# Kernel optimization log

Measured on AMD Instinct MI355X. Metric: run time of the kernel, lower is better.

The kernel has to match this reference:

```python
import jax, jax.numpy as jnp
import numpy as np

B, N, H, F, K = 64, 64, 256, 8, 2
E = N * (N - 1)


def _lin(k, fan_in, fan_out):
    return jax.random.normal(k, (fan_in, fan_out), jnp.float32) / np.sqrt(fan_in)


def setup_inputs() -> dict:
    key = jax.random.key(0)
    ks = jax.random.split(key, 20)
    # fully-connected directed edge list (no self loops), as in __init__
    idx = np.array([[i, j] for i in range(N) for j in range(N) if i != j], dtype=np.int64).T
    inp = {
        "inputs": jax.random.normal(ks[0], (B, N, F), jnp.float32),
        "hidden": jax.random.normal(ks[1], (B, N, H), jnp.float32),
        "edges": jax.random.uniform(ks[2], (E, K), jnp.float32),
        "edge_index": jnp.asarray(idx),
        # EdgeDecoder MLP: Linear(2H,2H) -> ELU -> Linear(2H,H)
        "ed_w1": _lin(ks[3], 2 * H, 2 * H), "ed_b1": jnp.full((2 * H,), 0.1, jnp.float32),
        "ed_w2": _lin(ks[4], 2 * H, H), "ed_b2": jnp.full((H,), 0.1, jnp.float32),
        # GRU-style hidden linears (no bias)
        "wr": _lin(ks[5], H, H), "wi": _lin(ks[6], H, H), "wh": _lin(ks[7], H, H),
        # input linears (with bias)
        "ir_w": _lin(ks[8], F, H), "ir_b": jnp.full((H,), 0.1, jnp.float32),
        "ii_w": _lin(ks[9], F, H), "ii_b": jnp.full((H,), 0.1, jnp.float32),
        "in_w": _lin(ks[10], F, H), "in_b": jnp.full((H,), 0.1, jnp.float32),
        # output MLP
        "f1_w": _lin(ks[11], H, H), "f1_b": jnp.full((H,), 0.1, jnp.float32),
        "f2_w": _lin(ks[12], H, H), "f2_b": jnp.full((H,), 0.1, jnp.float32),
        "f3_w": _lin(ks[13], H, F), "f3_b": jnp.full((F,), 0.1, jnp.float32),
    }
    return inp


def reference(inputs, hidden, edges, edge_index,
              ed_w1, ed_b1, ed_w2, ed_b2,
              wr, wi, wh,
              ir_w, ir_b, ii_w, ii_b, in_w, in_b,
              f1_w, f1_b, f2_w, f2_b, f3_w, f3_b):
    # convert_edge_index: max over edge-type dim -> per-edge scalar weight [E]
    w = jnp.max(edges, axis=-1)
    src, dst = edge_index[0], edge_index[1]   # PyG: x_j = x[src], x_i = x[dst]
    x_j = hidden[:, src]                      # [B,E,H] gather (irregular)
    x_i = hidden[:, dst]                      # [B,E,H]
    ef = jnp.concatenate([x_i, x_j], axis=-1) * w[None, :, None]   # [B,E,2H]
    # EdgeDecoder.mlp (dropout inactive in eval)
    m = jax.nn.elu(ef @ ed_w1 + ed_b1) @ ed_w2 + ed_b2             # [B,E,H]
    # mean-aggregate messages at receiver nodes (each node has N-1 in-edges)
    agg = jax.ops.segment_sum(m.transpose(1, 0, 2), dst, num_segments=N)
    agg = agg.transpose(1, 0, 2) / (N - 1)                         # [B,N,H]
    # GRU-style update
    r = jax.nn.sigmoid(inputs @ ir_w + ir_b + agg @ wr)
    i = jax.nn.sigmoid(inputs @ ii_w + ii_b + agg @ wi)
    n = jnp.tanh(inputs @ in_w + in_b + r * (agg @ wh))
    new_hidden = (1.0 - i) * n + i * hidden
    # output MLP with residual on inputs (dropout inactive in eval)
    pred = jax.nn.relu(new_hidden @ f1_w + f1_b)
    pred = jax.nn.relu(pred @ f2_w + f2_b)
    pred = inputs + (pred @ f3_w + f3_b)
    return pred, new_hidden
```

## Files before the change

kernel.cpp:

```cpp
#include <hip/hip_runtime.h>
#include <hip/hip_bf16.h>
#include <math.h>

#define BB 64
#define NN 64
#define HH 256
#define FF 8

typedef __bf16 bf16;
typedef bf16 bf16x2 __attribute__((ext_vector_type(2)));
typedef bf16 bf16x4 __attribute__((ext_vector_type(4)));
typedef bf16 bf16x8 __attribute__((ext_vector_type(8)));
typedef float f32x2 __attribute__((ext_vector_type(2)));
typedef float f32x4 __attribute__((ext_vector_type(4)));

#define GLL(g, l) __builtin_amdgcn_global_load_lds( \
    (const __attribute__((address_space(1))) void*)(g), \
    (__attribute__((address_space(3))) void*)(l), 16, 0, 0)

#define MFMA(a, b, c) __builtin_amdgcn_mfma_f32_16x16x32_bf16(a, b, c, 0, 0, 0)

#define WAITVM0 do { asm volatile("s_waitcnt vmcnt(0)" ::: "memory"); \
                     __builtin_amdgcn_sched_barrier(0); } while (0)
#define SBAR __builtin_amdgcn_sched_barrier(0)

__device__ __forceinline__ f32x2 unpk(unsigned int u) {
    union { unsigned int i; float f; } a, b;
    a.i = (u & 0xffffu) << 16;
    b.i = u & 0xffff0000u;
    f32x2 r; r.x = a.f; r.y = b.f; return r;
}

__device__ __forceinline__ bf16x8 frag128(const char* base, int row, int cbyte) {
    const int sw = (row & 7) << 4;
    const int a = row * 128 + cbyte;
    bf16x4 lo = *(const bf16x4*)(base + (a ^ sw));
    bf16x4 hi = *(const bf16x4*)(base + ((a + 32) ^ sw));
    return __builtin_shufflevector(lo, hi, 0, 1, 2, 3, 4, 5, 6, 7);
}

__device__ __forceinline__ bf16x8 frag512(const char* base, int row, int cbyte) {
    const int sw = (row & 7) << 4;
    const int a = row * 512 + cbyte;
    bf16x4 lo = *(const bf16x4*)(base + (a ^ sw));
    bf16x4 hi = *(const bf16x4*)(base + ((a + 32) ^ sw));
    return __builtin_shufflevector(lo, hi, 0, 1, 2, 3, 4, 5, 6, 7);
}

__device__ __forceinline__ bf16x8 frag1024(const char* base, int row, int cbyte) {
    const int sw = (row & 7) << 4;
    const int a = row * 1024 + cbyte;
    bf16x4 lo = *(const bf16x4*)(base + (a ^ sw));
    bf16x4 hi = *(const bf16x4*)(base + ((a + 32) ^ sw));
    return __builtin_shufflevector(lo, hi, 0, 1, 2, 3, 4, 5, 6, 7);
}

__device__ __forceinline__ void st512(char* base, int row, int col, bf16 v) {
    *(bf16*)(base + ((row * 512 + col * 2) ^ ((row & 7) << 4))) = v;
}

__global__ __launch_bounds__(256) void g1pack_kernel(
    const float* __restrict__ hidden, const float* __restrict__ ed_w1,
    const float* __restrict__ ed_w2,
    const float* __restrict__ wr, const float* __restrict__ wi,
    const float* __restrict__ wh,
    const float* __restrict__ f1_w, const float* __restrict__ f2_w,
    bf16* __restrict__ PQ, bf16* __restrict__ W2t, bf16* __restrict__ Wg,
    bf16* __restrict__ f1t, bf16* __restrict__ f2t)
{
    __shared__ __align__(1024) char smem[49408];
    const int tid = threadIdx.x;

    if (blockIdx.y >= 64) {
        const int t = (blockIdx.y - 64) * 16 + blockIdx.x;
        const float* src; bf16* dst; int R, C, tile;
        if (t < 32) { src = ed_w2; dst = W2t; R = 512; C = 256; tile = t; }
        else {
            int m = (t - 32) >> 4; tile = (t - 32) & 15; R = 256; C = 256;
            const float* ss[5] = {wr, wi, wh, f1_w, f2_w};
            bf16* dd[5] = {Wg, Wg + 65536, Wg + 131072, f1t, f2t};
            src = ss[m]; dst = dd[m];
        }
        const int tc = C >> 6;
        const int k0 = (tile / tc) * 64, n0 = (tile % tc) * 64;
        float (*ls)[65] = (float(*)[65])smem;
        {
            int rr = tid >> 2, cc = (tid & 3) * 16;
            const float* sp = src + (size_t)(k0 + rr) * C + n0 + cc;
#pragma unroll
            for (int j = 0; j < 16; j += 4) {
                float4 v = *(const float4*)(sp + j);
                ls[rr][cc + j] = v.x; ls[rr][cc + j + 1] = v.y;
                ls[rr][cc + j + 2] = v.z; ls[rr][cc + j + 3] = v.w;
            }
        }
        __syncthreads();
        {
            int n = tid >> 2, kc = (tid & 3) * 16;
            bf16x8 o0, o1;
#pragma unroll
            for (int j = 0; j < 8; ++j) o0[j] = (bf16)ls[kc + j][n];
#pragma unroll
            for (int j = 0; j < 8; ++j) o1[j] = (bf16)ls[kc + 8 + j][n];
            bf16* dp = dst + (size_t)(n0 + n) * R + k0 + kc;
            *(bf16x8*)dp = o0;
            *(bf16x8*)(dp + 8) = o1;
        }
        return;
    }

    char* Bs = smem;
    char* pool = smem + 32768;
    const int wave = tid >> 6, lane = tid & 63;
    const int wr_ = wave >> 1, wc_ = wave & 1;
    const int l15 = lane & 15, l4 = lane >> 4;
    const int bm = blockIdx.y * 64, bn = blockIdx.x * 64;
    const int roff = (bn >= 512) ? 256 : 0;
    const int ncol = bn & 511;

    {
        float (*ls)[65] = (float(*)[65])pool;
#pragma unroll
        for (int kt = 0; kt < 4; ++kt) {
            {
                int rr = tid >> 2, cc = (tid & 3) * 16;
                const float* sp = ed_w1 + (size_t)(kt * 64 + roff + rr) * 512 + ncol + cc;
#pragma unroll
                for (int j = 0; j < 16; j += 4) {
                    float4 v = *(const float4*)(sp + j);
                    ls[rr][cc + j] = v.x; ls[rr][cc + j + 1] = v.y;
                    ls[rr][cc + j + 2] = v.z; ls[rr][cc + j + 3] = v.w;
                }
            }
            __syncthreads();
            {
                int n = tid >> 2, kc = (tid & 3) * 16;
                bf16x8 o0, o1;
#pragma unroll
                for (int j = 0; j < 8; ++j) o0[j] = (bf16)ls[kc + j][n];
#pragma unroll
                for (int j = 0; j < 8; ++j) o1[j] = (bf16)ls[kc + 8 + j][n];
                int cb0 = kt * 8 + (kc >> 3);
                char* rowp = Bs + n * 512;
                *(bf16x8*)(rowp + ((cb0 ^ (n & 7)) * 16)) = o0;
                *(bf16x8*)(rowp + (((cb0 + 1) ^ (n & 7)) * 16)) = o1;
            }
            __syncthreads();
        }
    }

    f32x4 acc[2][2];
#pragma unroll
    for (int mf = 0; mf < 2; ++mf)
#pragma unroll
        for (int nf = 0; nf < 2; ++nf)
            acc[mf][nf] = (f32x4){0.f, 0.f, 0.f, 0.f};

    auto stageA = [&](int buf, int kt) {
        char* Ab = pool + buf * 8192;
#pragma unroll
        for (int a = 0; a < 2; ++a) {
            int idx = a * 256 + tid;
            int row = idx >> 3, cb = idx & 7;
            const float* gp = hidden + (size_t)(bm + row) * 256 + kt * 64 + cb * 8;
            float4 v0 = *(const float4*)gp;
            float4 v1 = *(const float4*)(gp + 4);
            bf16x8 o;
            o[0] = (bf16)v0.x; o[1] = (bf16)v0.y; o[2] = (bf16)v0.z; o[3] = (bf16)v0.w;
            o[4] = (bf16)v1.x; o[5] = (bf16)v1.y; o[6] = (bf16)v1.z; o[7] = (bf16)v1.w;
            *(bf16x8*)(Ab + row * 128 + ((cb ^ (row & 7)) * 16)) = o;
        }
    };

    auto computeT = [&](int buf, int kt) {
        char* Ab = pool + buf * 8192;
#pragma unroll
        for (int kk = 0; kk < 2; ++kk) {
            bf16x8 af[2];
#pragma unroll
            for (int mf = 0; mf < 2; ++mf)
                af[mf] = frag128(Ab, wr_ * 32 + mf * 16 + l15, kk * 64 + l4 * 8);
#pragma unroll
            for (int nf = 0; nf < 2; ++nf) {
                bf16x8 bfr = frag512(Bs, wc_ * 32 + nf * 16 + l15,
                                     kt * 128 + kk * 64 + l4 * 8);
#pragma unroll
                for (int mf = 0; mf < 2; ++mf)
                    acc[mf][nf] = MFMA(af[mf], bfr, acc[mf][nf]);
            }
        }
    };

    stageA(0, 0);
    __syncthreads();
#pragma unroll
    for (int t = 0; t < 4; ++t) {
        if (t < 3) stageA((t + 1) & 1, t + 1);
        computeT(t & 1, t);
        __syncthreads();
    }

#pragma unroll
    for (int mf = 0; mf < 2; ++mf)
#pragma unroll
        for (int nf = 0; nf < 2; ++nf)
#pragma unroll
            for (int r = 0; r < 4; ++r) {
                int grow = bm + wr_ * 32 + mf * 16 + l4 * 4 + r;
                int col = bn + wc_ * 32 + nf * 16 + l15;
                PQ[(size_t)grow * 1024 + col] = (bf16)acc[mf][nf][r];
            }
}

__global__ __launch_bounds__(1024) void fused_kernel(
    const bf16* __restrict__ PQ, const float* __restrict__ edges,
    const float* __restrict__ b1,
    const bf16* __restrict__ W2t, const float* __restrict__ ed_b2,
    const bf16* __restrict__ Wg,
    const bf16* __restrict__ f1t, const float* __restrict__ f1_b,
    const bf16* __restrict__ f2t, const float* __restrict__ f2_b,
    const float* __restrict__ f3_w, const float* __restrict__ f3_b,
    const float* __restrict__ inputs, const float* __restrict__ hidden,
    const float* __restrict__ irw, const float* __restrict__ irb,
    const float* __restrict__ iiw, const float* __restrict__ iib,
    const float* __restrict__ inw, const float* __restrict__ inb,
    float* __restrict__ NH, float* __restrict__ pred)
{
    __shared__ __align__(1024) char smem[65536];
    char* qs   = smem;
    char* bbase = smem;
    char* sl   = smem + 32768;
    float* f3s = (float*)(smem + 32768);
    char* h1l  = smem + 40960;
    float (*wls)[16] = (float(*)[16])(smem + 49152);
    char* aggl = smem + 49152;
    char* h2l  = smem + 49152;
    char* nhl  = smem + 57344;

    const int tid = threadIdx.x;
    const int wave = tid >> 6, lane = tid & 63;
    const int l15 = lane & 15, l4 = lane >> 4;
    const int srow = lane >> 3;
    const int scol = ((lane & 7) ^ (lane >> 3)) * 8;
    const int vb = (blockIdx.x & 7) * 32 + (blockIdx.x >> 3);
    const int b = vb >> 2, d0 = (vb & 3) * 16;
    const bf16* Pb = PQ + (size_t)(b * 64) * 1024;
    char* mybuf = bbase + wave * 2048;
    const int n0 = wave * 16;

    auto stageB = [&](const bf16* Wt, int Krow, int kt) {
#pragma unroll
        for (int s = 0; s < 2; ++s)
            GLL(Wt + (size_t)(n0 + s * 8 + srow) * Krow + kt * 64 + scol,
                mybuf + s * 1024 + lane * 16);
    };

#pragma unroll
    for (int si = 0; si < 2; ++si) {
        int row = wave * 2 + si;
        GLL(Pb + (size_t)row * 1024 + 512 + lane * 8, qs + row * 1024 + lane * 16);
    }
    {
        int src = tid >> 4, dc = tid & 15, d = d0 + dc;
        float w = 0.f;
        if (src != d) {
            int e = src * 63 + (d < src ? d : d - 1);
            float2 ev = ((const float2*)edges)[e];
            w = fmaxf(ev.x, ev.y);
        }
        wls[src][dc] = w;
    }
    const int c = tid & 255, hh = tid >> 8;
    f32x2 p2[4];
#pragma unroll
    for (int dd = 0; dd < 4; ++dd)
        p2[dd] = unpk(*(const unsigned int*)(Pb + (size_t)(d0 + hh * 4 + dd) * 1024 + 2 * c));
    float2 bbl = *(const float2*)(b1 + 2 * c);
    f32x2 bb; bb.x = bbl.x; bb.y = bbl.y;
    __syncthreads();

    f32x2 acc[4];
#pragma unroll
    for (int dd = 0; dd < 4; ++dd) acc[dd] = (f32x2){0.f, 0.f};
    const unsigned int* Qs32 = (const unsigned int*)qs;
    {
#pragma unroll 4
        for (int src = 0; src < 32; ++src) {
            f32x2 qv = unpk(Qs32[src * 256 + c]);
            float4 wv = *(const float4*)&wls[src][hh * 4];
            float w[4] = {wv.x, wv.y, wv.z, wv.w};
#pragma unroll
            for (int dd = 0; dd < 4; ++dd) {
                f32x2 w2v; w2v.x = w[dd]; w2v.y = w[dd];
                f32x2 v = (p2[dd] + qv) * w2v + bb;
                float e0 = __expf(v.x) - 1.f;
                float e1 = __expf(v.y) - 1.f;
                f32x2 r;
                r.x = (v.x > 0.f) ? v.x : e0;
                r.y = (v.y > 0.f) ? v.y : e1;
                acc[dd] += r;
            }
        }
    }
    __syncthreads();
#pragma unroll
    for (int si = 0; si < 2; ++si) {
        int row = wave * 2 + si;
        GLL(Pb + (size_t)(32 + row) * 1024 + 512 + lane * 8,
            qs + row * 1024 + lane * 16);
    }
    __syncthreads();
    {
#pragma unroll 4
        for (int src = 32; src < 64; ++src) {
            f32x2 qv = unpk(Qs32[(src - 32) * 256 + c]);
            float4 wv = *(const float4*)&wls[src][hh * 4];
            float w[4] = {wv.x, wv.y, wv.z, wv.w};
#pragma unroll
            for (int dd = 0; dd < 4; ++dd) {
                f32x2 w2v; w2v.x = w[dd]; w2v.y = w[dd];
                f32x2 v = (p2[dd] + qv) * w2v + bb;
                float e0 = __expf(v.x) - 1.f;
                float e1 = __expf(v.y) - 1.f;
                f32x2 r;
                r.x = (v.x > 0.f) ? v.x : e0;
                r.y = (v.y > 0.f) ? v.y : e1;
                acc[dd] += r;
            }
        }
        f32x2 selfc;
        selfc.x = (bb.x > 0.f) ? bb.x : (__expf(bb.x) - 1.f);
        selfc.y = (bb.y > 0.f) ? bb.y : (__expf(bb.y) - 1.f);
#pragma unroll
        for (int dd = 0; dd < 4; ++dd) {
            int row = hh * 4 + dd;
            bf16x2 st;
            st[0] = (bf16)(acc[dd].x - selfc.x);
            st[1] = (bf16)(acc[dd].y - selfc.y);
            *(bf16x2*)(sl + ((row * 1024 + 4 * c) ^ ((row & 7) << 4))) = st;
        }
    }
    __syncthreads();

    {
        f32x4 a1 = (f32x4){0.f, 0.f, 0.f, 0.f};
#pragma unroll
        for (int kt = 0; kt < 8; ++kt) {
            SBAR; stageB(W2t, 512, kt); WAITVM0;
#pragma unroll
            for (int kk = 0; kk < 2; ++kk) {
                bf16x8 af = frag1024(sl, l15, kt * 128 + kk * 64 + l4 * 8);
                a1 = MFMA(af, frag128(mybuf, l15, kk * 64 + l4 * 8), a1);
            }
        }
        int col = n0 + l15;
        float eb = ed_b2[col];
#pragma unroll
        for (int r = 0; r < 4; ++r)
            st512(aggl, l4 * 4 + r, col, (bf16)(a1[r] * (1.f / 63.f) + eb));
    }
    __syncthreads();

    for (int i = tid; i < 2048; i += 1024) f3s[i] = f3_w[i];

    {
        f32x4 a2[3];
#pragma unroll
        for (int g = 0; g < 3; ++g) a2[g] = (f32x4){0.f, 0.f, 0.f, 0.f};
#pragma unroll
        for (int st_ = 0; st_ < 12; ++st_) {
            const int g = st_ >> 2, kt = st_ & 3;
            SBAR; stageB(Wg + (size_t)g * 65536, 256, kt); WAITVM0;
#pragma unroll
            for (int kk = 0; kk < 2; ++kk) {
                bf16x8 af = frag512(aggl, l15, kt * 128 + kk * 64 + l4 * 8);
                a2[g] = MFMA(af, frag128(mybuf, l15, kk * 64 + l4 * 8), a2[g]);
            }
        }
        const int col = n0 + l15;
        float w8r[8], w8i[8], w8n[8];
#pragma unroll
        for (int f = 0; f < 8; ++f) {
            w8r[f] = irw[f * 256 + col];
            w8i[f] = iiw[f * 256 + col];
            w8n[f] = inw[f * 256 + col];
        }
        const float xr0 = irb[col], xi0 = iib[col], xn0 = inb[col];
#pragma unroll
        for (int r = 0; r < 4; ++r) {
            const int lrow = l4 * 4 + r;
            const int grow = b * 64 + d0 + lrow;
            const float* inp = inputs + (size_t)grow * 8;
            float xr = xr0, xi = xi0, xn = xn0;
#pragma unroll
            for (int f = 0; f < 8; ++f) {
                float x = inp[f];
                xr += x * w8r[f]; xi += x * w8i[f]; xn += x * w8n[f];
            }
            float aR = a2[0][r];
            float aI = a2[1][r];
            float aN = a2[2][r];
            float rg = __builtin_amdgcn_rcpf(1.f + __expf(-(xr + aR)));
            float ig = __builtin_amdgcn_rcpf(1.f + __expf(-(xi + aI)));
            float tz = xn + rg * aN;
            tz = fminf(fmaxf(tz, -15.f), 15.f);
            float e2x = __expf(2.f * tz);
            float nn = (e2x - 1.f) * __builtin_amdgcn_rcpf(e2x + 1.f);
            size_t o = (size_t)grow * 256 + col;
            float nh = (1.f - ig) * nn + ig * hidden[o];
            NH[o] = nh;
            st512(nhl, lrow, col, (bf16)nh);
        }
    }
    __syncthreads();

    {
        f32x4 a1 = (f32x4){0.f, 0.f, 0.f, 0.f};
#pragma unroll
        for (int kt = 0; kt < 4; ++kt) {
            SBAR; stageB(f1t, 256, kt); WAITVM0;
#pragma unroll
            for (int kk = 0; kk < 2; ++kk) {
                bf16x8 af = frag512(nhl, l15, kt * 128 + kk * 64 + l4 * 8);
                a1 = MFMA(af, frag128(mybuf, l15, kk * 64 + l4 * 8), a1);
            }
        }
        int col = n0 + l15;
        float bv = f1_b[col];
#pragma unroll
        for (int r = 0; r < 4; ++r)
            st512(h1l, l4 * 4 + r, col, (bf16)fmaxf(a1[r] + bv, 0.f));
    }
    __syncthreads();

    {
        f32x4 a1 = (f32x4){0.f, 0.f, 0.f, 0.f};
#pragma unroll
        for (int kt = 0; kt < 4; ++kt) {
            SBAR; stageB(f2t, 256, kt); WAITVM0;
#pragma unroll
            for (int kk = 0; kk < 2; ++kk) {
                bf16x8 af = frag512(h1l, l15, kt * 128 + kk * 64 + l4 * 8);
                a1 = MFMA(af, frag128(mybuf, l15, kk * 64 + l4 * 8), a1);
            }
        }
        int col = n0 + l15;
        float bv = f2_b[col];
#pragma unroll
        for (int r = 0; r < 4; ++r)
            st512(h2l, l4 * 4 + r, col, (bf16)fmaxf(a1[r] + bv, 0.f));
    }
    __syncthreads();

    if (tid < 128) {
        const int row = tid >> 3, f = tid & 7;
        const int sw = (row & 7) << 4;
        float a = f3_b[f];
        for (int k0 = 0; k0 < 256; k0 += 8) {
            bf16x8 h8 = *(const bf16x8*)(h2l + ((row * 512 + k0 * 2) ^ sw));
#pragma unroll
            for (int j = 0; j < 8; ++j)
                a += (float)h8[j] * f3s[(k0 + j) * 8 + f];
        }
        int gi = (b * 64 + d0 + row) * 8 + f;
        pred[gi] = inputs[gi] + a;
    }
}

extern "C" void kernel_launch(void* const* d_in, const int* in_sizes, int n_in,
                              void* d_out, int out_size, void* d_ws, size_t ws_size,
                              hipStream_t stream) {
    const float* inputs = (const float*)d_in[0];
    const float* hidden = (const float*)d_in[1];
    const float* edges  = (const float*)d_in[2];
    const float* ed_w1 = (const float*)d_in[4];
    const float* ed_b1 = (const float*)d_in[5];
    const float* ed_w2 = (const float*)d_in[6];
    const float* ed_b2 = (const float*)d_in[7];
    const float* wr = (const float*)d_in[8];
    const float* wi = (const float*)d_in[9];
    const float* wh = (const float*)d_in[10];
    const float* ir_w = (const float*)d_in[11];
    const float* ir_b = (const float*)d_in[12];
    const float* ii_w = (const float*)d_in[13];
    const float* ii_b = (const float*)d_in[14];
    const float* in_w = (const float*)d_in[15];
    const float* in_b = (const float*)d_in[16];
    const float* f1_w = (const float*)d_in[17];
    const float* f1_b = (const float*)d_in[18];
    const float* f2_w = (const float*)d_in[19];
    const float* f2_b = (const float*)d_in[20];
    const float* f3_w = (const float*)d_in[21];
    const float* f3_b = (const float*)d_in[22];

    float* out = (float*)d_out;
    float* pred = out;
    float* NH = out + (size_t)BB * NN * FF;

    bf16* bws = (bf16*)d_ws;
    bf16* PQ   = bws;
    bf16* W2t  = bws + 4194304;
    bf16* Wg   = bws + 4325376;
    bf16* f1t  = bws + 4521984;
    bf16* f2t  = bws + 4587520;

    g1pack_kernel<<<dim3(16, 71), dim3(256), 0, stream>>>(
        hidden, ed_w1, ed_w2, wr, wi, wh, f1_w, f2_w,
        PQ, W2t, Wg, f1t, f2t);

    fused_kernel<<<dim3(256), dim3(1024), 0, stream>>>(
        PQ, edges, ed_b1, W2t, ed_b2, Wg, f1t, f1_b, f2t, f2_b,
        f3_w, f3_b, inputs, hidden,
        ir_w, ir_b, ii_w, ii_b, in_w, in_b, NH, pred);
}
```

Measured before the change: 66.87 us.

## Split edge aggregation into its own kernel with finer-grained blocks

Moves the per-edge ELU message accumulation out of the fused kernel into a separate kernel of 1024 blocks of 256 threads, each handling 4 destination nodes. It writes the aggregated pre-activation sums to a bf16 workspace that the GRU/MLP kernel then loads via global-to-LDS copies. The intent is more parallelism and occupancy for the exp-heavy aggregation phase, which previously ran on only 256 large blocks. The cost is an extra kernel launch and a global round trip of the intermediate buffer.

```diff
diff --git a/kernel.cpp b/kernel.cpp
--- a/kernel.cpp
+++ b/kernel.cpp
@@ -212,9 +212,75 @@
             }
 }
 
-__global__ __launch_bounds__(1024) void fused_kernel(
+__global__ __launch_bounds__(256) void edge_agg_kernel(
     const bf16* __restrict__ PQ, const float* __restrict__ edges,
-    const float* __restrict__ b1,
+    const float* __restrict__ b1, bf16* __restrict__ S)
+{
+    const int blk0 = blockIdx.x;
+    const int vb = (blk0 & 7) * 128 + (blk0 >> 3);
+    const int dgrp = vb & 15;
+    const int b = vb >> 4;
+    const int tid = threadIdx.x;
+    const int d0 = dgrp * 4;
+
+    __shared__ __align__(16) float wls[64][4];
+    {
+        int src = tid >> 2, dd = tid & 3;
+        int d = d0 + dd;
+        float w = 0.f;
+        if (src != d) {
+            int e = src * 63 + (d < src ? d : d - 1);
+            float2 ev = ((const float2*)edges)[e];
+            w = fmaxf(ev.x, ev.y);
+        }
+        wls[src][dd] = w;
+    }
+    __syncthreads();
+
+    const bf16* Pb = PQ + (size_t)(b * 64) * 1024;
+    f32x2 p2[4];
+#pragma unroll
+    for (int dd = 0; dd < 4; ++dd)
+        p2[dd] = unpk(*(const unsigned int*)(Pb + (size_t)(d0 + dd) * 1024 + 2 * tid));
+    float2 bbl = *(const float2*)(b1 + 2 * tid);
+    f32x2 bb; bb.x = bbl.x; bb.y = bbl.y;
+    const unsigned int* Qp = (const unsigned int*)(Pb + 512) + tid;
+
+    f32x2 acc[4];
+#pragma unroll
+    for (int dd = 0; dd < 4; ++dd) acc[dd] = (f32x2){0.f, 0.f};
+
+#pragma unroll 4
+    for (int src = 0; src < 64; ++src) {
+        f32x2 q = unpk(Qp[(size_t)src * 512]);
+        float4 wv = *(const float4*)&wls[src][0];
+        float w[4] = {wv.x, wv.y, wv.z, wv.w};
+#pragma unroll
+        for (int dd = 0; dd < 4; ++dd) {
+            f32x2 w2; w2.x = w[dd]; w2.y = w[dd];
+            f32x2 v = (p2[dd] + q) * w2 + bb;
+            float e0 = __expf(v.x) - 1.f;
+            float e1 = __expf(v.y) - 1.f;
+            f32x2 r;
+            r.x = (v.x > 0.f) ? v.x : e0;
+            r.y = (v.y > 0.f) ? v.y : e1;
+            acc[dd] += r;
+        }
+    }
+    f32x2 selfc;
+    selfc.x = (bb.x > 0.f) ? bb.x : (__expf(bb.x) - 1.f);
+    selfc.y = (bb.y > 0.f) ? bb.y : (__expf(bb.y) - 1.f);
+#pragma unroll
+    for (int dd = 0; dd < 4; ++dd) {
+        bf16x2 st;
+        st[0] = (bf16)(acc[dd].x - selfc.x);
+        st[1] = (bf16)(acc[dd].y - selfc.y);
+        *(bf16x2*)(S + (size_t)(b * 64 + d0 + dd) * 512 + 2 * tid) = st;
+    }
+}
+
+__global__ __launch_bounds__(1024) void gru_mlp_kernel(
+    const bf16* __restrict__ Sb,
     const bf16* __restrict__ W2t, const float* __restrict__ ed_b2,
     const bf16* __restrict__ Wg,
     const bf16* __restrict__ f1t, const float* __restrict__ f1_b,
@@ -227,12 +293,10 @@
     float* __restrict__ NH, float* __restrict__ pred)
 {
     __shared__ __align__(1024) char smem[65536];
-    char* qs   = smem;
     char* bbase = smem;
     char* sl   = smem + 32768;
     float* f3s = (float*)(smem + 32768);
     char* h1l  = smem + 40960;
-    float (*wls)[16] = (float(*)[16])(smem + 49152);
     char* aggl = smem + 49152;
     char* h2l  = smem + 49152;
     char* nhl  = smem + 57344;
@@ -244,7 +308,6 @@
     const int scol = ((lane & 7) ^ (lane >> 3)) * 8;
     const int vb = (blockIdx.x & 7) * 32 + (blockIdx.x >> 3);
     const int b = vb >> 2, d0 = (vb & 3) * 16;
-    const bf16* Pb = PQ + (size_t)(b * 64) * 1024;
     char* mybuf = bbase + wave * 2048;
     const int n0 = wave * 16;
 
@@ -255,90 +318,10 @@
                 mybuf + s * 1024 + lane * 16);
     };
 
-#pragma unroll
-    for (int si = 0; si < 2; ++si) {
-        int row = wave * 2 + si;
-        GLL(Pb + (size_t)row * 1024 + 512 + lane * 8, qs + row * 1024 + lane * 16);
-    }
-    {
-        int src = tid >> 4, dc = tid & 15, d = d0 + dc;
-        float w = 0.f;
-        if (src != d) {
-            int e = src * 63 + (d < src ? d : d - 1);
-            float2 ev = ((const float2*)edges)[e];
-            w = fmaxf(ev.x, ev.y);
-        }
-        wls[src][dc] = w;
-    }
-    const int c = tid & 255, hh = tid >> 8;
-    f32x2 p2[4];
-#pragma unroll
-    for (int dd = 0; dd < 4; ++dd)
-        p2[dd] = unpk(*(const unsigned int*)(Pb + (size_t)(d0 + hh * 4 + dd) * 1024 + 2 * c));
-    float2 bbl = *(const float2*)(b1 + 2 * c);
-    f32x2 bb; bb.x = bbl.x; bb.y = bbl.y;
-    __syncthreads();
-
-    f32x2 acc[4];
-#pragma unroll
-    for (int dd = 0; dd < 4; ++dd) acc[dd] = (f32x2){0.f, 0.f};
-    const unsigned int* Qs32 = (const unsigned int*)qs;
-    {
-#pragma unroll 4
-        for (int src = 0; src < 32; ++src) {
-            f32x2 qv = unpk(Qs32[src * 256 + c]);
-            float4 wv = *(const float4*)&wls[src][hh * 4];
-            float w[4] = {wv.x, wv.y, wv.z, wv.w};
-#pragma unroll
-            for (int dd = 0; dd < 4; ++dd) {
-                f32x2 w2v; w2v.x = w[dd]; w2v.y = w[dd];
-                f32x2 v = (p2[dd] + qv) * w2v + bb;
-                float e0 = __expf(v.x) - 1.f;
-                float e1 = __expf(v.y) - 1.f;
-                f32x2 r;
-                r.x = (v.x > 0.f) ? v.x : e0;
-                r.y = (v.y > 0.f) ? v.y : e1;
-                acc[dd] += r;
-            }
-        }
-    }
-    __syncthreads();
-#pragma unroll
-    for (int si = 0; si < 2; ++si) {
-        int row = wave * 2 + si;
-        GLL(Pb + (size_t)(32 + row) * 1024 + 512 + lane * 8,
-            qs + row * 1024 + lane * 16);
-    }
-    __syncthreads();
-    {
-#pragma unroll 4
-        for (int src = 32; src < 64; ++src) {
-            f32x2 qv = unpk(Qs32[(src - 32) * 256 + c]);
-            float4 wv = *(const float4*)&wls[src][hh * 4];
-            float w[4] = {wv.x, wv.y, wv.z, wv.w};
-#pragma unroll
-            for (int dd = 0; dd < 4; ++dd) {
-                f32x2 w2v; w2v.x = w[dd]; w2v.y = w[dd];
-                f32x2 v = (p2[dd] + qv) * w2v + bb;
-                float e0 = __expf(v.x) - 1.f;
-                float e1 = __expf(v.y) - 1.f;
-                f32x2 r;
-                r.x = (v.x > 0.f) ? v.x : e0;
-                r.y = (v.y > 0.f) ? v.y : e1;
-                acc[dd] += r;
-            }
-        }
-        f32x2 selfc;
-        selfc.x = (bb.x > 0.f) ? bb.x : (__expf(bb.x) - 1.f);
-        selfc.y = (bb.y > 0.f) ? bb.y : (__expf(bb.y) - 1.f);
-#pragma unroll
-        for (int dd = 0; dd < 4; ++dd) {
-            int row = hh * 4 + dd;
-            bf16x2 st;
-            st[0] = (bf16)(acc[dd].x - selfc.x);
-            st[1] = (bf16)(acc[dd].y - selfc.y);
-            *(bf16x2*)(sl + ((row * 1024 + 4 * c) ^ ((row & 7) << 4))) = st;
-        }
+    {
+        const int row = wave;
+        GLL(Sb + (size_t)(b * 64 + d0 + row) * 512 + ((lane ^ (row & 7)) * 8),
+            sl + row * 1024 + lane * 16);
     }
     __syncthreads();
 
@@ -503,13 +486,16 @@
     bf16* Wg   = bws + 4325376;
     bf16* f1t  = bws + 4521984;
     bf16* f2t  = bws + 4587520;
+    bf16* Sb   = bws + 4653056;
 
     g1pack_kernel<<<dim3(16, 71), dim3(256), 0, stream>>>(
         hidden, ed_w1, ed_w2, wr, wi, wh, f1_w, f2_w,
         PQ, W2t, Wg, f1t, f2t);
 
-    fused_kernel<<<dim3(256), dim3(1024), 0, stream>>>(
-        PQ, edges, ed_b1, W2t, ed_b2, Wg, f1t, f1_b, f2t, f2_b,
+    edge_agg_kernel<<<dim3(1024), dim3(256), 0, stream>>>(PQ, edges, ed_b1, Sb);
+
+    gru_mlp_kernel<<<dim3(256), dim3(1024), 0, stream>>>(
+        Sb, W2t, ed_b2, Wg, f1t, f1_b, f2t, f2_b,
         f3_w, f3_b, inputs, hidden,
         ir_w, ir_b, ii_w, ii_b, in_w, in_b, NH, pred);
 }
```

Result: slower. 71.76 us (+7.3%).
